# Kernel tuning notes

Hardware: AMD Instinct MI355X
Metric: run time of the kernel (lower is better)

## Reference

```python
import jax, jax.numpy as jnp
import numpy as np

KH, KW = 3, 3
STRIDE, PAD, DIL = 1, 1, 1


def setup_inputs() -> dict:
    key = jax.random.key(0)
    k1, k2, k3 = jax.random.split(key, 3)
    B, C, H, W, O = 8, 128, 64, 64, 128
    x = jax.random.normal(k1, (B, C, H, W), jnp.float32)
    # offset layout: [B, 2*K, Ho, Wo], pairs (dy, dx) per kernel tap
    offset = jax.random.normal(k2, (B, 2 * KH * KW, H, W), jnp.float32)
    n = C * KH * KW
    stdv = 1.0 / np.sqrt(n)
    weight = jax.random.uniform(k3, (O, C, KH, KW), jnp.float32, -stdv, stdv)
    bias = jnp.zeros((O,), jnp.float32)
    return {"x": x, "offset": offset, "weight": weight, "bias": bias}


def _deform_conv(x, offset, weight, bias):
    B, C, H, W = x.shape
    O = weight.shape[0]
    K = KH * KW
    Ho = (H + 2 * PAD - DIL * (KH - 1) - 1) // STRIDE + 1
    Wo = (W + 2 * PAD - DIL * (KW - 1) - 1) // STRIDE + 1

    off = offset.reshape(B, K, 2, Ho, Wo)  # (dy, dx) per tap

    # base sampling grid for each kernel tap: [K, Ho, Wo]
    hs = jnp.arange(Ho, dtype=jnp.float32) * STRIDE - PAD
    ws = jnp.arange(Wo, dtype=jnp.float32) * STRIDE - PAD
    ki = jnp.arange(KH, dtype=jnp.float32) * DIL
    kj = jnp.arange(KW, dtype=jnp.float32) * DIL
    base_y = (ki[:, None, None, None] + hs[None, None, :, None])  # [KH,1,Ho,1]
    base_x = (kj[None, :, None, None] + ws[None, None, None, :])  # [1,KW,1,Wo]
    base_y = jnp.broadcast_to(base_y, (KH, KW, Ho, Wo)).reshape(K, Ho, Wo)
    base_x = jnp.broadcast_to(base_x, (KH, KW, Ho, Wo)).reshape(K, Ho, Wo)

    py = base_y[None] + off[:, :, 0]  # [B,K,Ho,Wo]
    px = base_x[None] + off[:, :, 1]

    y0 = jnp.floor(py)
    x0 = jnp.floor(px)
    ly = py - y0  # fractional parts
    lx = px - x0
    y0i = y0.astype(jnp.int32)
    x0i = x0.astype(jnp.int32)

    flat = x.reshape(B, C, H * W)

    def gather(yi, xi, w):
        # zero outside the image (DCN zero-padding semantics)
        valid = (yi >= 0) & (yi < H) & (xi >= 0) & (xi < W)
        idx = jnp.clip(yi, 0, H - 1) * W + jnp.clip(xi, 0, W - 1)  # [B,K,Ho,Wo]
        g = jnp.take_along_axis(flat, idx.reshape(B, 1, -1), axis=2)
        g = g.reshape(B, C, K, Ho, Wo)
        wmask = (w * valid.astype(x.dtype))[:, None]  # [B,1,K,Ho,Wo]
        return g * wmask

    # bilinear accumulation over 4 corners -> im2col columns [B,C,K,Ho,Wo]
    cols = gather(y0i, x0i, (1 - ly) * (1 - lx))
    cols = cols + gather(y0i, x0i + 1, (1 - ly) * lx)
    cols = cols + gather(y0i + 1, x0i, ly * (1 - lx))
    cols = cols + gather(y0i + 1, x0i + 1, ly * lx)

    out = jnp.einsum('ock,bckhw->bohw', weight.reshape(O, C, K), cols)
    return out + bias[None, :, None, None]


def reference(x, offset, weight, bias):
    return _deform_conv(x, offset, weight, bias)
```

## Files before the change

### kernel.cpp

```cpp
#include <hip/hip_runtime.h>


#define BB 8
#define CC 128
#define HH 64
#define WW 64
#define OO 128
#define KTAPS 9

typedef __attribute__((ext_vector_type(8))) short bf16x8;
typedef __attribute__((ext_vector_type(4))) float f32x4;

__device__ __forceinline__ unsigned short f2bf(float f) {
    unsigned u = __float_as_uint(f);
    u += 0x7FFFu + ((u >> 16) & 1u);
    return (unsigned short)(u >> 16);
}
#if __has_builtin(__builtin_amdgcn_cvt_pk_bf16_f32)
typedef __attribute__((ext_vector_type(2))) __bf16 bf16x2_t;
__device__ __forceinline__ unsigned pack2bf(float lo, float hi) {
    bf16x2_t v = __builtin_amdgcn_cvt_pk_bf16_f32(lo, hi);
    unsigned r;
    __builtin_memcpy(&r, &v, 4);
    return r;
}
#else
__device__ __forceinline__ unsigned pack2bf(float lo, float hi) {
    return (unsigned)f2bf(lo) | ((unsigned)f2bf(hi) << 16);
}
#endif
__device__ __forceinline__ float bflo(unsigned p) { return __uint_as_float(p << 16); }
__device__ __forceinline__ float bfhi(unsigned p) { return __uint_as_float(p & 0xFFFF0000u); }

__global__ __launch_bounds__(256)
void prep_kernel(const float* __restrict__ x, const float* __restrict__ wgt,
                 unsigned short* __restrict__ xt, unsigned short* __restrict__ wpk) {
    const int t = threadIdx.x;
    if (blockIdx.x < 512) {
        __shared__ float tile[WW * 132];
        const int b = blockIdx.x >> 6;
        const int h = blockIdx.x & 63;
        const float* src = x + ((size_t)b * CC * HH + h) * WW;
        {
            const int wq = t & 15;
            const int cb = t >> 4;
#pragma unroll
            for (int it = 0; it < 8; ++it) {
                const int c = it * 16 + cb;
                const float4 v = *reinterpret_cast<const float4*>(src + (size_t)c * (HH * WW) + wq * 4);
                tile[(wq * 4 + 0) * 132 + c] = v.x;
                tile[(wq * 4 + 1) * 132 + c] = v.y;
                tile[(wq * 4 + 2) * 132 + c] = v.z;
                tile[(wq * 4 + 3) * 132 + c] = v.w;
            }
        }
        __syncthreads();
        unsigned short* dst = xt + ((size_t)b * HH + h) * WW * CC;
        {
            const int cg = t & 15;
            const int wb = t >> 4;
#pragma unroll
            for (int it = 0; it < 4; ++it) {
                const int w = it * 16 + wb;
                const float* tp = &tile[w * 132 + cg * 8];
                uint4 p;
                p.x = pack2bf(tp[0], tp[1]);
                p.y = pack2bf(tp[2], tp[3]);
                p.z = pack2bf(tp[4], tp[5]);
                p.w = pack2bf(tp[6], tp[7]);
                *reinterpret_cast<uint4*>(&dst[(size_t)w * CC + cg * 8]) = p;
            }
        }
    } else {
        const int id   = (blockIdx.x - 512) * 256 + t;
        const int lane = id & 63;
        const int frag = id >> 6;
        const int nt   = frag & 7;
        const int c0q  = (frag >> 3) & 3;
        const int tap  = frag >> 5;
        const int o    = (nt << 4) + (lane & 15);
        const int c    = (c0q << 5) + ((lane >> 4) << 3);
        const float* s = wgt + ((size_t)o * CC + c) * KTAPS + tap;
        unsigned u[4];
#pragma unroll
        for (int j = 0; j < 4; ++j)
            u[j] = pack2bf(s[(2 * j) * KTAPS], s[(2 * j + 1) * KTAPS]);
        *reinterpret_cast<uint4*>(wpk + (size_t)frag * 512 + lane * 8) =
            make_uint4(u[0], u[1], u[2], u[3]);
    }
}

__device__ __forceinline__ void decode_tap(const float2* __restrict__ sLL,
                                           const short2* __restrict__ sYX,
                                           int rec, int extra,
                                           unsigned& o00, unsigned& o01,
                                           unsigned& o10, unsigned& o11,
                                           float& w00, float& w01,
                                           float& w10, float& w11) {
    const float2 ll = sLL[rec];
    const short2 yx = sYX[rec];
    const int y0 = yx.x, x0 = yx.y;
    const int y1 = y0 + 1, x1 = x0 + 1;
    const float ly = ll.x, lx = ll.y;
    const bool vy0 = ((unsigned)y0 < (unsigned)HH);
    const bool vy1 = ((unsigned)y1 < (unsigned)HH);
    const bool vx0 = ((unsigned)x0 < (unsigned)WW);
    const bool vx1 = ((unsigned)x1 < (unsigned)WW);
    w00 = (vy0 && vx0) ? (1.f - ly) * (1.f - lx) : 0.f;
    w01 = (vy0 && vx1) ? (1.f - ly) * lx         : 0.f;
    w10 = (vy1 && vx0) ? ly * (1.f - lx)         : 0.f;
    w11 = (vy1 && vx1) ? ly * lx                 : 0.f;
    const int cy0 = min(max(y0, 0), HH - 1);
    const int cy1 = min(max(y1, 0), HH - 1);
    const int cx0 = min(max(x0, 0), WW - 1);
    const int cx1 = min(max(x1, 0), WW - 1);
    o00 = (unsigned)((((cy0 << 6) + cx0) << 8) + extra);
    o01 = (unsigned)((((cy0 << 6) + cx1) << 8) + extra);
    o10 = (unsigned)((((cy1 << 6) + cx0) << 8) + extra);
    o11 = (unsigned)((((cy1 << 6) + cx1) << 8) + extra);
}

__global__ __launch_bounds__(512, 4)
void dcn_mfma_kernel(const unsigned short* __restrict__ xt,
                     const unsigned short* __restrict__ wpk,
                     const float* __restrict__ offset,
                     const float* __restrict__ bias,
                     float* __restrict__ out) {
    __shared__ __align__(16) float smem_f[4 * 128 * 20];
    float2* sLL = reinterpret_cast<float2*>(smem_f);
    short2* sYX = reinterpret_cast<short2*>(smem_f + 1152);

    const int t = threadIdx.x;
    const int bid0 = blockIdx.x;
    const int nid  = ((bid0 & 7) << 6) | (bid0 >> 3);
    const int b    = nid >> 6;
    const int ho   = nid & 63;

    for (int s = t; s < KTAPS * 64; s += 512) {
        const int k  = s >> 6;
        const int wo = s & 63;
        const int ki = k / 3;
        const int kj = k - ki * 3;
        const float dy = offset[(((size_t)b * 18 + 2 * k    ) * 64 + ho) * 64 + wo];
        const float dx = offset[(((size_t)b * 18 + 2 * k + 1) * 64 + ho) * 64 + wo];
        const float py = (float)(ho - 1 + ki) + dy;
        const float px = (float)(wo - 1 + kj) + dx;
        const float y0f = floorf(py);
        const float x0f = floorf(px);
        sLL[s] = make_float2(py - y0f, px - x0f);
        sYX[s] = make_short2((short)(int)y0f, (short)(int)x0f);
    }
    __syncthreads();

    f32x4 acc[8];
#pragma unroll
    for (int nt = 0; nt < 8; ++nt) acc[nt] = (f32x4){0.f, 0.f, 0.f, 0.f};

    const int lane = t & 63;
    const int wave = t >> 6;
    const int mt   = wave & 3;
    const int grp  = wave >> 2;
    const int lm   = lane & 15;
    const int quad = lane >> 4;
    const int lane16 = lane * 16;
    const int extra = (grp << 7) + (quad << 4);
    const char* xb = (const char*)(xt + (size_t)b * HH * WW * CC);
    const char* wb = (const char*)wpk;
    const int fb_grp = grp << 1;

    unsigned o00, o01, o10, o11;
    float w00, w01, w10, w11;
    decode_tap(sLL, sYX, (mt << 4) + lm, extra, o00, o01, o10, o11, w00, w01, w10, w11);
    uint4 a00 = *reinterpret_cast<const uint4*>(xb + o00);
    uint4 a01 = *reinterpret_cast<const uint4*>(xb + o01);
    uint4 a10 = *reinterpret_cast<const uint4*>(xb + o10);
    uint4 a11 = *reinterpret_cast<const uint4*>(xb + o11);

    for (int tap = 0; tap < KTAPS; ++tap) {
#pragma unroll
        for (int cq = 0; cq < 2; ++cq) {
            uint4 bfr[8];
            const int fragbase = (((tap << 2) + fb_grp + cq)) << 3;
            const char* wrow = wb + ((size_t)fragbase << 10) + lane16;
#pragma unroll
            for (int nt = 0; nt < 8; ++nt)
                bfr[nt] = *reinterpret_cast<const uint4*>(wrow + (nt << 10));

            uint4 n00, n01, n10, n11;
            unsigned no00 = 0, no01 = 0, no10 = 0, no11 = 0;
            float nw00 = 0.f, nw01 = 0.f, nw10 = 0.f, nw11 = 0.f;
            if (cq == 0) {
                n00 = *reinterpret_cast<const uint4*>(xb + o00 + 64);
                n01 = *reinterpret_cast<const uint4*>(xb + o01 + 64);
                n10 = *reinterpret_cast<const uint4*>(xb + o10 + 64);
                n11 = *reinterpret_cast<const uint4*>(xb + o11 + 64);
            } else if (tap < KTAPS - 1) {
                decode_tap(sLL, sYX, ((tap + 1) << 6) + (mt << 4) + lm, extra,
                           no00, no01, no10, no11, nw00, nw01, nw10, nw11);
                n00 = *reinterpret_cast<const uint4*>(xb + no00);
                n01 = *reinterpret_cast<const uint4*>(xb + no01);
                n10 = *reinterpret_cast<const uint4*>(xb + no10);
                n11 = *reinterpret_cast<const uint4*>(xb + no11);
            }

            const unsigned* u00 = reinterpret_cast<const unsigned*>(&a00);
            const unsigned* u01 = reinterpret_cast<const unsigned*>(&a01);
            const unsigned* u10 = reinterpret_cast<const unsigned*>(&a10);
            const unsigned* u11 = reinterpret_cast<const unsigned*>(&a11);
            unsigned afu[4];
#pragma unroll
            for (int j = 0; j < 4; ++j) {
                const float rl = w00 * bflo(u00[j]) + w01 * bflo(u01[j])
                               + w10 * bflo(u10[j]) + w11 * bflo(u11[j]);
                const float rh = w00 * bfhi(u00[j]) + w01 * bfhi(u01[j])
                               + w10 * bfhi(u10[j]) + w11 * bfhi(u11[j]);
                afu[j] = pack2bf(rl, rh);
            }
            bf16x8 afrag;
            __builtin_memcpy(&afrag, afu, 16);
#pragma unroll
            for (int nt = 0; nt < 8; ++nt) {
                bf16x8 bfrag;
                __builtin_memcpy(&bfrag, &bfr[nt], 16);
                acc[nt] = __builtin_amdgcn_mfma_f32_16x16x32_bf16(afrag, bfrag, acc[nt], 0, 0, 0);
            }

            if (cq == 0) {
                a00 = n00; a01 = n01; a10 = n10; a11 = n11;
            } else if (tap < KTAPS - 1) {
                a00 = n00; a01 = n01; a10 = n10; a11 = n11;
                o00 = no00; o01 = no01; o10 = no10; o11 = no11;
                w00 = nw00; w01 = nw01; w10 = nw10; w11 = nw11;
            }
        }
    }

    __syncthreads();
    float* scrM = smem_f + mt * (128 * 20);
    if (grp == 0) {
#pragma unroll
        for (int nt = 0; nt < 8; ++nt) {
            const int o_l = (nt << 4) + lm;
            *reinterpret_cast<float4*>(&scrM[o_l * 20 + (quad << 2)]) =
                make_float4(acc[nt][0], acc[nt][1], acc[nt][2], acc[nt][3]);
        }
    }
    __syncthreads();
    if (grp == 1) {
#pragma unroll
        for (int nt = 0; nt < 8; ++nt) {
            const int o_l = (nt << 4) + lm;
            float4* p = reinterpret_cast<float4*>(&scrM[o_l * 20 + (quad << 2)]);
            float4 f = *p;
            f.x += acc[nt][0]; f.y += acc[nt][1];
            f.z += acc[nt][2]; f.w += acc[nt][3];
            *p = f;
        }
    }
    __syncthreads();
    {
        const int o = (grp << 6) + lane;
        const float bv = bias[o];
        float* op = out + (((size_t)(b * OO + o) * HH + ho) << 6) + (mt << 4);
        const float* sr = scrM + o * 20;
#pragma unroll
        for (int j = 0; j < 4; ++j) {
            const float4 f = *reinterpret_cast<const float4*>(sr + j * 4);
            *reinterpret_cast<float4*>(op + j * 4) =
                make_float4(f.x + bv, f.y + bv, f.z + bv, f.w + bv);
        }
    }
}

extern "C" void kernel_launch(void* const* d_in, const int* in_sizes, int n_in,
                              void* d_out, int out_size, void* d_ws, size_t ws_size,
                              hipStream_t stream) {
    const float* x      = (const float*)d_in[0];
    const float* offset = (const float*)d_in[1];
    const float* wgt    = (const float*)d_in[2];
    const float* bias   = (const float*)d_in[3];
    float* out = (float*)d_out;

    unsigned short* xt  = (unsigned short*)d_ws;
    unsigned short* wpk = xt + (size_t)BB * HH * WW * CC;

    hipLaunchKernelGGL(prep_kernel, dim3(512 + 72), dim3(256), 0, stream, x, wgt, xt, wpk);
    hipLaunchKernelGGL(dcn_mfma_kernel, dim3(BB * HH), dim3(512), 0, stream,
                       xt, wpk, offset, bias, out);
}
```

Before: 131.4 us.

## Stage per-tap weight fragments in double-buffered LDS via async global-to-LDS loads

Weight fragments for each tap (32 KB) are copied from global memory into a double-buffered LDS region with global_load_lds, and the next tap is prefetched while the current one is consumed. MFMA B operands are then read from LDS instead of global/L2. The aim is to remove repeated global weight reads across the 8 waves and hide their latency. In exchange it adds a block-wide barrier every tap and raises LDS use to about 72 KB per block, which may cut occupancy below the requested 4 blocks per CU.

```diff
diff --git a/kernel.cpp b/kernel.cpp
--- a/kernel.cpp
+++ b/kernel.cpp
@@ -31,6 +31,20 @@
 #endif
 __device__ __forceinline__ float bflo(unsigned p) { return __uint_as_float(p << 16); }
 __device__ __forceinline__ float bfhi(unsigned p) { return __uint_as_float(p & 0xFFFF0000u); }
+
+__device__ __forceinline__ void gload_lds16(const void* g, void* l) {
+#if __has_builtin(__builtin_amdgcn_global_load_lds)
+    auto* lp = reinterpret_cast<__attribute__((address_space(3))) unsigned*>(
+        reinterpret_cast<uintptr_t>(l));
+    auto* gp = reinterpret_cast<const __attribute__((address_space(1))) unsigned*>(
+        reinterpret_cast<uintptr_t>(g));
+    __builtin_amdgcn_global_load_lds(gp, lp, 16, 0, 0);
+#else
+    const int lane = threadIdx.x & 63;
+    *reinterpret_cast<uint4*>(reinterpret_cast<char*>(l) + lane * 16) =
+        *reinterpret_cast<const uint4*>(reinterpret_cast<const char*>(g) + lane * 16);
+#endif
+}
 
 __global__ __launch_bounds__(256)
 void prep_kernel(const float* __restrict__ x, const float* __restrict__ wgt,
@@ -126,15 +140,28 @@
                      const float* __restrict__ offset,
                      const float* __restrict__ bias,
                      float* __restrict__ out) {
-    __shared__ __align__(16) float smem_f[4 * 128 * 20];
-    float2* sLL = reinterpret_cast<float2*>(smem_f);
-    short2* sYX = reinterpret_cast<short2*>(smem_f + 1152);
+    __shared__ __align__(16) char smem[6912 + 2 * 32768];
+    float2* sLL = reinterpret_cast<float2*>(smem);
+    short2* sYX = reinterpret_cast<short2*>(smem + 4608);
+    char*   Bb  = smem + 6912;
 
     const int t = threadIdx.x;
     const int bid0 = blockIdx.x;
     const int nid  = ((bid0 & 7) << 6) | (bid0 >> 3);
     const int b    = nid >> 6;
     const int ho   = nid & 63;
+
+    const int lane = t & 63;
+    const int wave = t >> 6;
+    const int mt   = wave & 3;
+    const int grp  = wave >> 2;
+    const int lm   = lane & 15;
+    const int quad = lane >> 4;
+    const int lane16 = lane * 16;
+    const int extra = (grp << 7) + (quad << 4);
+    const char* xb = (const char*)(xt + (size_t)b * HH * WW * CC);
+    const char* wb = (const char*)wpk;
+    const int fb_grp = grp << 1;
 
     for (int s = t; s < KTAPS * 64; s += 512) {
         const int k  = s >> 6;
@@ -150,23 +177,19 @@
         sLL[s] = make_float2(py - y0f, px - x0f);
         sYX[s] = make_short2((short)(int)y0f, (short)(int)x0f);
     }
+
+    {
+        const char* src = wb + wave * 4096 + lane16;
+        char* dst = Bb + wave * 4096;
+#pragma unroll
+        for (int j = 0; j < 4; ++j)
+            gload_lds16(src + j * 1024, dst + j * 1024);
+    }
     __syncthreads();
 
     f32x4 acc[8];
 #pragma unroll
     for (int nt = 0; nt < 8; ++nt) acc[nt] = (f32x4){0.f, 0.f, 0.f, 0.f};
-
-    const int lane = t & 63;
-    const int wave = t >> 6;
-    const int mt   = wave & 3;
-    const int grp  = wave >> 2;
-    const int lm   = lane & 15;
-    const int quad = lane >> 4;
-    const int lane16 = lane * 16;
-    const int extra = (grp << 7) + (quad << 4);
-    const char* xb = (const char*)(xt + (size_t)b * HH * WW * CC);
-    const char* wb = (const char*)wpk;
-    const int fb_grp = grp << 1;
 
     unsigned o00, o01, o10, o11;
     float w00, w01, w10, w11;
@@ -176,15 +199,24 @@
     uint4 a10 = *reinterpret_cast<const uint4*>(xb + o10);
     uint4 a11 = *reinterpret_cast<const uint4*>(xb + o11);
 
+    int cur = 0;
     for (int tap = 0; tap < KTAPS; ++tap) {
+        if (tap < KTAPS - 1) {
+            const char* src = wb + (tap + 1) * 32768 + wave * 4096 + lane16;
+            char* dst = Bb + ((cur ^ 1) << 15) + wave * 4096;
+#pragma unroll
+            for (int j = 0; j < 4; ++j)
+                gload_lds16(src + j * 1024, dst + j * 1024);
+        }
+
+        const char* bslice = Bb + (cur << 15);
 #pragma unroll
         for (int cq = 0; cq < 2; ++cq) {
             uint4 bfr[8];
-            const int fragbase = (((tap << 2) + fb_grp + cq)) << 3;
-            const char* wrow = wb + ((size_t)fragbase << 10) + lane16;
+            const char* brow = bslice + (((fb_grp + cq) << 13) + lane16);
 #pragma unroll
             for (int nt = 0; nt < 8; ++nt)
-                bfr[nt] = *reinterpret_cast<const uint4*>(wrow + (nt << 10));
+                bfr[nt] = *reinterpret_cast<const uint4*>(brow + (nt << 10));
 
             uint4 n00, n01, n10, n11;
             unsigned no00 = 0, no01 = 0, no10 = 0, no11 = 0;
@@ -233,10 +265,13 @@
                 w00 = nw00; w01 = nw01; w10 = nw10; w11 = nw11;
             }
         }
-    }
-
-    __syncthreads();
-    float* scrM = smem_f + mt * (128 * 20);
+
+        __syncthreads();
+        cur ^= 1;
+    }
+
+    float* scrA = reinterpret_cast<float*>(Bb);
+    float* scrM = scrA + mt * (128 * 20);
     if (grp == 0) {
 #pragma unroll
         for (int nt = 0; nt < 8; ++nt) {
```

Measured after the change: 121.9 us. 7.2% less time.
